# Kernel optimization log

Measured on AMD Instinct MI355X. Metric: run time of the kernel, lower is better.

The kernel has to match this reference:

```python
import jax, jax.numpy as jnp
import numpy as np

E, H, I, K, BLK = 16, 2048, 2048, 4, 32
ALPHA, LIMIT = 1.702, 7.0
T = 1024


def setup_inputs() -> dict:
    key = jax.random.key(0)
    ks = jax.random.split(key, 12)
    f32 = jnp.float32
    return {
        "hidden_states": jax.random.normal(ks[0], (T, H), f32),
        "router_weight": jax.random.normal(ks[1], (E, H), f32) * 0.02,
        "router_bias": jax.random.normal(ks[2], (E,), f32) * 0.02,
        "gate_blocks": jax.random.normal(ks[3], (E, I, H // BLK, BLK), f32),
        "gate_scales": jax.random.uniform(ks[4], (E, I, H // BLK), f32, 0.01, 0.04),
        "gate_bias": jax.random.normal(ks[5], (E, I), f32) * 0.02,
        "up_blocks": jax.random.normal(ks[6], (E, I, H // BLK, BLK), f32),
        "up_scales": jax.random.uniform(ks[7], (E, I, H // BLK), f32, 0.01, 0.04),
        "up_bias": jax.random.normal(ks[8], (E, I), f32) * 0.02,
        "down_blocks": jax.random.normal(ks[9], (E, H, I // BLK, BLK), f32),
        "down_scales": jax.random.uniform(ks[10], (E, H, I // BLK), f32, 0.01, 0.04),
        "down_bias": jax.random.normal(ks[11], (E, H), f32) * 0.02,
    }


def reference(hidden_states, router_weight, router_bias,
              gate_blocks, gate_scales, gate_bias,
              up_blocks, up_scales, up_bias,
              down_blocks, down_scales, down_bias):
    x = hidden_states.reshape(-1, H)              # [T, H]
    t = x.shape[0]

    # --- router: top-k + softmax over top-k, scattered to dense scores ---
    logits = x @ router_weight.T + router_bias    # [T, E]
    topv, topi = jax.lax.top_k(logits, K)         # [T, K]
    topv = jax.nn.softmax(topv, axis=-1)
    scores = jnp.zeros((t, E), x.dtype).at[jnp.arange(t)[:, None], topi].set(topv)

    # --- inline block (mxfp4-style) dequantization: blocks * per-block scale ---
    gate_w = (gate_blocks * gate_scales[..., None]).reshape(E, I, H)
    up_w = (up_blocks * up_scales[..., None]).reshape(E, I, H)
    down_w = (down_blocks * down_scales[..., None]).reshape(E, H, I)

    # --- GptOss GLU experts ---
    g = jnp.einsum('th,eih->eti', x, gate_w) + gate_bias[:, None, :]   # [E, T, I]
    u = jnp.einsum('th,eih->eti', x, up_w) + up_bias[:, None, :]
    g = jnp.minimum(g, LIMIT)
    u = jnp.clip(u, -LIMIT, LIMIT)
    glu = g * jax.nn.sigmoid(g * ALPHA)
    h = (u + 1.0) * glu                                                # [E, T, I]
    o = jnp.einsum('eti,ehi->eth', h, down_w) + down_bias[:, None, :]  # [E, T, H]

    # --- weighted combine by routing scores (zero for unrouted experts) ---
    out = jnp.einsum('eth,te->th', o, scores)
    return out
```

## Files before the change

kernel.cpp:

```cpp
#include <hip/hip_runtime.h>


#define HD 2048
#define ID 2048
#define NE 16
#define NT 1024
#define NTOPK 4
#define NSLOTS (NT * NTOPK)

typedef unsigned short u16;
typedef __attribute__((ext_vector_type(8))) short short8;
typedef __attribute__((ext_vector_type(4))) float f32x4;

__device__ __forceinline__ float bf2f(u16 v) {
    return __uint_as_float(((unsigned)v) << 16);
}
__device__ __forceinline__ u16 f2bf(float f) {
    unsigned u = __float_as_uint(f);
    return (u16)((u + 0x7fffu + ((u >> 16) & 1u)) >> 16);
}

__global__ void router_kernel(const float* __restrict__ x,
                              const float* __restrict__ rw,
                              const float* __restrict__ rb,
                              u16* __restrict__ xb,
                              int* __restrict__ counts,
                              int* __restrict__ topi,
                              float* __restrict__ topv) {
    const int t = blockIdx.x;
    const int lane = threadIdx.x;

    float xr[32];
#pragma unroll
    for (int j = 0; j < 32; ++j) xr[j] = x[(size_t)t * HD + j * 64 + lane];
#pragma unroll
    for (int j = 0; j < 32; ++j) xb[(size_t)t * HD + j * 64 + lane] = f2bf(xr[j]);

    float lg[NE];
#pragma unroll
    for (int e = 0; e < NE; ++e) {
        const float* w = rw + (size_t)e * HD;
        float s = 0.f;
#pragma unroll
        for (int j = 0; j < 32; ++j) s = fmaf(xr[j], w[j * 64 + lane], s);
        for (int off = 32; off > 0; off >>= 1) s += __shfl_xor(s, off);
        lg[e] = s + rb[e];
    }

    if (lane == 0) {
        unsigned used = 0;
        float sv[NTOPK];
        int si[NTOPK];
#pragma unroll
        for (int k = 0; k < NTOPK; ++k) {
            float best = -1e30f;
            int bi = 0;
#pragma unroll
            for (int e = 0; e < NE; ++e) {
                if (!(used & (1u << e)) && lg[e] > best) { best = lg[e]; bi = e; }
            }
            used |= 1u << bi;
            sv[k] = best;
            si[k] = bi;
        }
        const float mx = sv[0];
        float p[NTOPK], sum = 0.f;
#pragma unroll
        for (int k = 0; k < NTOPK; ++k) { p[k] = __expf(sv[k] - mx); sum += p[k]; }
        const float inv = 1.0f / sum;
#pragma unroll
        for (int k = 0; k < NTOPK; ++k) {
            atomicAdd(&counts[si[k]], 1);
            topi[t * NTOPK + k] = si[k];
            topv[t * NTOPK + k] = p[k] * inv;
        }
    }
}

__global__ void bases_kernel(const int* __restrict__ counts, int* __restrict__ bases) {
    if (threadIdx.x == 0) {
        int acc = 0;
#pragma unroll
        for (int e = 0; e < NE; ++e) { bases[e] = acc; acc += counts[e]; }
    }
}

__global__ void assign_kernel(const int* __restrict__ topi, const float* __restrict__ topv,
                              const int* __restrict__ bases, int* __restrict__ cursor,
                              int* __restrict__ tok_slot, float* __restrict__ wgt_slot) {
    const int t = blockIdx.x * 256 + threadIdx.x;
    if (t < NT) {
#pragma unroll
        for (int k = 0; k < NTOPK; ++k) {
            const int e = topi[t * NTOPK + k];
            const int s = atomicAdd(&cursor[e], 1);
            const int slot = bases[e] + s;
            tok_slot[slot] = t;
            wgt_slot[slot] = topv[t * NTOPK + k];
        }
    }
}

__global__ __launch_bounds__(256, 2) void gu_gemm(
    const u16* __restrict__ xb,
    const float* __restrict__ gate_blocks, const float* __restrict__ gate_scales,
    const float* __restrict__ gate_bias,
    const float* __restrict__ up_blocks, const float* __restrict__ up_scales,
    const float* __restrict__ up_bias,
    const int* __restrict__ counts, const int* __restrict__ bases,
    const int* __restrict__ tok_slot,
    u16* __restrict__ gbuf, u16* __restrict__ ubuf) {
    const int e = blockIdx.z >> 1, mat = blockIdx.z & 1;
    const int n_e = counts[e];
    const int mt = blockIdx.y;
    if (mt * 256 >= n_e) return;
    const int rows = min(256, n_e - mt * 256);
    const int base = bases[e] + mt * 256;
    const float* wb = mat ? up_blocks : gate_blocks;
    const float* wsc = mat ? up_scales : gate_scales;
    const float* wbias = mat ? up_bias : gate_bias;
    u16* outb = mat ? ubuf : gbuf;
    const int n0 = blockIdx.x * 64;

    __shared__ __align__(16) short Asl[4][256][8];
    __shared__ __align__(16) short Bsl[4][64][8];

    const int tid = threadIdx.x;
    const int wave = tid >> 6, lane = tid & 63;

    const int tokA = tok_slot[base + min(tid, rows - 1)];
    const u16* aptr = xb + (size_t)tokA * HD;
    const int bn = tid & 63, bq = tid >> 6;
    const float* bptr = wb + ((size_t)e * ID + n0 + bn) * HD + bq * 8;
    const float* sptr = wsc + ((size_t)e * ID + n0 + bn) * (HD / 32);

    f32x4 acc[4][4];
#pragma unroll
    for (int a = 0; a < 4; ++a)
#pragma unroll
        for (int b = 0; b < 4; ++b) acc[a][b] = (f32x4){0.f, 0.f, 0.f, 0.f};

    int4 areg0, areg1, areg2, areg3;
    float4 br0, br1;
    float sreg;
    {
        const int4* ap = (const int4*)aptr;
        areg0 = ap[0]; areg1 = ap[1]; areg2 = ap[2]; areg3 = ap[3];
        const float4* bp = (const float4*)bptr;
        br0 = bp[0]; br1 = bp[1];
        sreg = sptr[0];
    }

    for (int kb = 0; kb < 64; ++kb) {
        __syncthreads();
        *(int4*)&Asl[0][tid][0] = areg0;
        *(int4*)&Asl[1][tid][0] = areg1;
        *(int4*)&Asl[2][tid][0] = areg2;
        *(int4*)&Asl[3][tid][0] = areg3;
        {
            const int p0 = (int)((unsigned)f2bf(br0.x * sreg) | ((unsigned)f2bf(br0.y * sreg) << 16));
            const int p1 = (int)((unsigned)f2bf(br0.z * sreg) | ((unsigned)f2bf(br0.w * sreg) << 16));
            const int p2 = (int)((unsigned)f2bf(br1.x * sreg) | ((unsigned)f2bf(br1.y * sreg) << 16));
            const int p3 = (int)((unsigned)f2bf(br1.z * sreg) | ((unsigned)f2bf(br1.w * sreg) << 16));
            *(int4*)&Bsl[bq][bn][0] = make_int4(p0, p1, p2, p3);
        }
        __syncthreads();
        if (kb < 63) {
            const int4* ap = (const int4*)(aptr + (kb + 1) * 32);
            areg0 = ap[0]; areg1 = ap[1]; areg2 = ap[2]; areg3 = ap[3];
            const float4* bp = (const float4*)(bptr + (kb + 1) * 32);
            br0 = bp[0]; br1 = bp[1];
            sreg = sptr[kb + 1];
        }
        const int kch = lane >> 4, lr = lane & 15;
        short8 af[4], bfv[4];
#pragma unroll
        for (int mi = 0; mi < 4; ++mi)
            af[mi] = *(const short8*)&Asl[kch][wave * 64 + mi * 16 + lr][0];
#pragma unroll
        for (int ni = 0; ni < 4; ++ni)
            bfv[ni] = *(const short8*)&Bsl[kch][ni * 16 + lr][0];
#pragma unroll
        for (int mi = 0; mi < 4; ++mi)
#pragma unroll
            for (int ni = 0; ni < 4; ++ni)
                acc[mi][ni] = __builtin_amdgcn_mfma_f32_16x16x32_bf16(af[mi], bfv[ni], acc[mi][ni], 0, 0, 0);
    }

    const int lr = lane & 15, qq = lane >> 4;
#pragma unroll
    for (int ni = 0; ni < 4; ++ni) {
        const int col = n0 + ni * 16 + lr;
        const float bv = wbias[e * ID + col];
#pragma unroll
        for (int mi = 0; mi < 4; ++mi)
#pragma unroll
            for (int j = 0; j < 4; ++j) {
                const int ml = wave * 64 + mi * 16 + qq * 4 + j;
                if (ml < rows) outb[(size_t)(base + ml) * ID + col] = f2bf(acc[mi][ni][j] + bv);
            }
    }
}

__global__ void act_kernel(const u16* __restrict__ g, const u16* __restrict__ u,
                           u16* __restrict__ h) {
    const size_t i = (size_t)blockIdx.x * 256 + threadIdx.x;
    const int4 gv = ((const int4*)g)[i];
    const int4 uv = ((const int4*)u)[i];
    const int gi[4] = {gv.x, gv.y, gv.z, gv.w};
    const int ui[4] = {uv.x, uv.y, uv.z, uv.w};
    int hi[4];
#pragma unroll
    for (int c = 0; c < 4; ++c) {
        float res[2];
#pragma unroll
        for (int p = 0; p < 2; ++p) {
            float gg = bf2f((u16)(((unsigned)gi[c] >> (16 * p)) & 0xffffu));
            float uu = bf2f((u16)(((unsigned)ui[c] >> (16 * p)) & 0xffffu));
            gg = fminf(gg, 7.0f);
            uu = fminf(fmaxf(uu, -7.0f), 7.0f);
            const float sig = 1.0f / (1.0f + __expf(-1.702f * gg));
            res[p] = (uu + 1.0f) * (gg * sig);
        }
        hi[c] = (int)((unsigned)f2bf(res[0]) | ((unsigned)f2bf(res[1]) << 16));
    }
    ((int4*)h)[i] = make_int4(hi[0], hi[1], hi[2], hi[3]);
}

__global__ __launch_bounds__(256, 2) void down_gemm(
    const u16* __restrict__ hbuf,
    const float* __restrict__ down_blocks, const float* __restrict__ down_scales,
    const float* __restrict__ down_bias,
    const int* __restrict__ counts, const int* __restrict__ bases,
    const int* __restrict__ tok_slot, const float* __restrict__ wgt_slot,
    float* __restrict__ out) {
    const int e = blockIdx.z;
    const int n_e = counts[e];
    const int mt = blockIdx.y;
    if (mt * 256 >= n_e) return;
    const int rows = min(256, n_e - mt * 256);
    const int base = bases[e] + mt * 256;
    const int n0 = blockIdx.x * 64;

    __shared__ __align__(16) short Asl[4][256][8];
    __shared__ __align__(16) short Bsl[4][64][8];

    const int tid = threadIdx.x;
    const int wave = tid >> 6, lane = tid & 63;

    const int slotA = min(base + tid, NSLOTS - 1);
    const u16* aptr = hbuf + (size_t)slotA * ID;
    const int bn = tid & 63, bq = tid >> 6;
    const float* bptr = down_blocks + ((size_t)e * HD + n0 + bn) * ID + bq * 8;
    const float* sptr = down_scales + ((size_t)e * HD + n0 + bn) * (ID / 32);

    f32x4 acc[4][4];
#pragma unroll
    for (int a = 0; a < 4; ++a)
#pragma unroll
        for (int b = 0; b < 4; ++b) acc[a][b] = (f32x4){0.f, 0.f, 0.f, 0.f};

    int4 areg0, areg1, areg2, areg3;
    float4 br0, br1;
    float sreg;
    {
        const int4* ap = (const int4*)aptr;
        areg0 = ap[0]; areg1 = ap[1]; areg2 = ap[2]; areg3 = ap[3];
        const float4* bp = (const float4*)bptr;
        br0 = bp[0]; br1 = bp[1];
        sreg = sptr[0];
    }

    for (int kb = 0; kb < 64; ++kb) {
        __syncthreads();
        *(int4*)&Asl[0][tid][0] = areg0;
        *(int4*)&Asl[1][tid][0] = areg1;
        *(int4*)&Asl[2][tid][0] = areg2;
        *(int4*)&Asl[3][tid][0] = areg3;
        {
            const int p0 = (int)((unsigned)f2bf(br0.x * sreg) | ((unsigned)f2bf(br0.y * sreg) << 16));
            const int p1 = (int)((unsigned)f2bf(br0.z * sreg) | ((unsigned)f2bf(br0.w * sreg) << 16));
            const int p2 = (int)((unsigned)f2bf(br1.x * sreg) | ((unsigned)f2bf(br1.y * sreg) << 16));
            const int p3 = (int)((unsigned)f2bf(br1.z * sreg) | ((unsigned)f2bf(br1.w * sreg) << 16));
            *(int4*)&Bsl[bq][bn][0] = make_int4(p0, p1, p2, p3);
        }
        __syncthreads();
        if (kb < 63) {
            const int4* ap = (const int4*)(aptr + (kb + 1) * 32);
            areg0 = ap[0]; areg1 = ap[1]; areg2 = ap[2]; areg3 = ap[3];
            const float4* bp = (const float4*)(bptr + (kb + 1) * 32);
            br0 = bp[0]; br1 = bp[1];
            sreg = sptr[kb + 1];
        }
        const int kch = lane >> 4, lr = lane & 15;
        short8 af[4], bfv[4];
#pragma unroll
        for (int mi = 0; mi < 4; ++mi)
            af[mi] = *(const short8*)&Asl[kch][wave * 64 + mi * 16 + lr][0];
#pragma unroll
        for (int ni = 0; ni < 4; ++ni)
            bfv[ni] = *(const short8*)&Bsl[kch][ni * 16 + lr][0];
#pragma unroll
        for (int mi = 0; mi < 4; ++mi)
#pragma unroll
            for (int ni = 0; ni < 4; ++ni)
                acc[mi][ni] = __builtin_amdgcn_mfma_f32_16x16x32_bf16(af[mi], bfv[ni], acc[mi][ni], 0, 0, 0);
    }

    const int lr = lane & 15, qq = lane >> 4;
    float bvs[4];
#pragma unroll
    for (int ni = 0; ni < 4; ++ni) bvs[ni] = down_bias[e * HD + n0 + ni * 16 + lr];
#pragma unroll
    for (int mi = 0; mi < 4; ++mi)
#pragma unroll
        for (int j = 0; j < 4; ++j) {
            const int ml = wave * 64 + mi * 16 + qq * 4 + j;
            if (ml >= rows) continue;
            const int slot = base + ml;
            const int tok = tok_slot[slot];
            const float wg = wgt_slot[slot];
            float* orow = out + (size_t)tok * HD;
#pragma unroll
            for (int ni = 0; ni < 4; ++ni)
                atomicAdd(&orow[n0 + ni * 16 + lr], wg * (acc[mi][ni][j] + bvs[ni]));
        }
}

extern "C" void kernel_launch(void* const* d_in, const int* in_sizes, int n_in,
                              void* d_out, int out_size, void* d_ws, size_t ws_size,
                              hipStream_t stream) {
    const float* x           = (const float*)d_in[0];
    const float* rw          = (const float*)d_in[1];
    const float* rb          = (const float*)d_in[2];
    const float* gate_blocks = (const float*)d_in[3];
    const float* gate_scales = (const float*)d_in[4];
    const float* gate_bias   = (const float*)d_in[5];
    const float* up_blocks   = (const float*)d_in[6];
    const float* up_scales   = (const float*)d_in[7];
    const float* up_bias     = (const float*)d_in[8];
    const float* down_blocks = (const float*)d_in[9];
    const float* down_scales = (const float*)d_in[10];
    const float* down_bias   = (const float*)d_in[11];
    float* out = (float*)d_out;

    char* ws = (char*)d_ws;
    u16* xb     = (u16*)ws;
    u16* gbuf   = (u16*)(ws + (4 << 20));
    u16* ubuf   = (u16*)(ws + (20 << 20));
    u16* hbuf   = (u16*)(ws + (36 << 20));
    int* counts = (int*)(ws + (52 << 20));
    int* cursor = counts + 16;
    int* basesp = counts + 32;
    int* topi   = counts + 64;
    float* topv = (float*)(counts + 64 + 4096);
    int* tok_slot = (int*)(counts + 64 + 8192);
    float* wgt_slot = (float*)(counts + 64 + 12288);

    hipMemsetAsync(d_out, 0, (size_t)NT * HD * sizeof(float), stream);
    hipMemsetAsync(counts, 0, 128, stream);

    router_kernel<<<NT, 64, 0, stream>>>(x, rw, rb, xb, counts, topi, topv);
    bases_kernel<<<1, 64, 0, stream>>>(counts, basesp);
    assign_kernel<<<NT / 256, 256, 0, stream>>>(topi, topv, basesp, cursor, tok_slot, wgt_slot);
    gu_gemm<<<dim3(ID / 64, 4, NE * 2), 256, 0, stream>>>(
        xb, gate_blocks, gate_scales, gate_bias, up_blocks, up_scales, up_bias,
        counts, basesp, tok_slot, gbuf, ubuf);
    act_kernel<<<(NSLOTS * ID / 8) / 256, 256, 0, stream>>>(gbuf, ubuf, hbuf);
    down_gemm<<<dim3(HD / 64, 4, NE), 256, 0, stream>>>(
        hbuf, down_blocks, down_scales, down_bias, counts, basesp, tok_slot, wgt_slot, out);
}
```

Baseline: 1.525 ms.

## Load A fragments directly from global and double-buffer dequantized B in LDS

Result: faster. 1.279 ms (-16.1%).

```diff
diff --git a/kernel.cpp b/kernel.cpp
--- a/kernel.cpp
+++ b/kernel.cpp
@@ -122,17 +122,23 @@
     u16* outb = mat ? ubuf : gbuf;
     const int n0 = blockIdx.x * 64;
 
-    __shared__ __align__(16) short Asl[4][256][8];
-    __shared__ __align__(16) short Bsl[4][64][8];
+    __shared__ __align__(16) short Bsl[2][8][64][8];
 
     const int tid = threadIdx.x;
     const int wave = tid >> 6, lane = tid & 63;
-
-    const int tokA = tok_slot[base + min(tid, rows - 1)];
-    const u16* aptr = xb + (size_t)tokA * HD;
-    const int bn = tid & 63, bq = tid >> 6;
-    const float* bptr = wb + ((size_t)e * ID + n0 + bn) * HD + bq * 8;
-    const float* sptr = wsc + ((size_t)e * ID + n0 + bn) * (HD / 32);
+    const int lr = lane & 15, kch = lane >> 4;
+
+    const u16* ap[4];
+#pragma unroll
+    for (int mi = 0; mi < 4; ++mi) {
+        const int m = wave * 64 + mi * 16 + lr;
+        const int tok = tok_slot[base + min(m, rows - 1)];
+        ap[mi] = xb + (size_t)tok * HD + kch * 8;
+    }
+
+    const int col = tid & 63, q = tid >> 6;
+    const float* bptr = wb + ((size_t)e * ID + n0 + col) * HD + q * 16;
+    const float* sptr = wsc + ((size_t)e * ID + n0 + col) * (HD / 32);
 
     f32x4 acc[4][4];
 #pragma unroll
@@ -140,64 +146,78 @@
 #pragma unroll
         for (int b = 0; b < 4; ++b) acc[a][b] = (f32x4){0.f, 0.f, 0.f, 0.f};
 
-    int4 areg0, areg1, areg2, areg3;
-    float4 br0, br1;
-    float sreg;
-    {
-        const int4* ap = (const int4*)aptr;
-        areg0 = ap[0]; areg1 = ap[1]; areg2 = ap[2]; areg3 = ap[3];
-        const float4* bp = (const float4*)bptr;
-        br0 = bp[0]; br1 = bp[1];
-        sreg = sptr[0];
-    }
-
-    for (int kb = 0; kb < 64; ++kb) {
+    float4 br0, br1, br2, br3;
+    float sc;
+#define LOADB(KB)                                                    \
+    {                                                                \
+        const float4* p = (const float4*)(bptr + (KB) * 64);         \
+        br0 = p[0]; br1 = p[1]; br2 = p[2]; br3 = p[3];              \
+        sc = sptr[(KB) * 2 + (q >> 1)];                              \
+    }
+#define WRITEB(BUF)                                                  \
+    {                                                                \
+        short8 lo, hi;                                               \
+        lo[0] = (short)f2bf(br0.x * sc); lo[1] = (short)f2bf(br0.y * sc); \
+        lo[2] = (short)f2bf(br0.z * sc); lo[3] = (short)f2bf(br0.w * sc); \
+        lo[4] = (short)f2bf(br1.x * sc); lo[5] = (short)f2bf(br1.y * sc); \
+        lo[6] = (short)f2bf(br1.z * sc); lo[7] = (short)f2bf(br1.w * sc); \
+        hi[0] = (short)f2bf(br2.x * sc); hi[1] = (short)f2bf(br2.y * sc); \
+        hi[2] = (short)f2bf(br2.z * sc); hi[3] = (short)f2bf(br2.w * sc); \
+        hi[4] = (short)f2bf(br3.x * sc); hi[5] = (short)f2bf(br3.y * sc); \
+        hi[6] = (short)f2bf(br3.z * sc); hi[7] = (short)f2bf(br3.w * sc); \
+        *(short8*)&Bsl[BUF][q * 2][col][0] = lo;                     \
+        *(short8*)&Bsl[BUF][q * 2 + 1][col][0] = hi;                 \
+    }
+
+    LOADB(0);
+    WRITEB(0);
+    LOADB(1);
+    __syncthreads();
+
+    for (int kb = 0; kb < 32; ++kb) {
+        short8 a0[4], a1[4];
+#pragma unroll
+        for (int mi = 0; mi < 4; ++mi) {
+            a0[mi] = *(const short8*)(ap[mi] + kb * 64);
+            a1[mi] = *(const short8*)(ap[mi] + kb * 64 + 32);
+        }
+        if (kb + 1 < 32) {
+            WRITEB((kb + 1) & 1);
+            if (kb + 2 < 32) LOADB(kb + 2);
+        }
+        const int buf = kb & 1;
+        short8 bfv[2][4];
+#pragma unroll
+        for (int s = 0; s < 2; ++s)
+#pragma unroll
+            for (int ni = 0; ni < 4; ++ni)
+                bfv[s][ni] = *(const short8*)&Bsl[buf][s * 4 + kch][ni * 16 + lr][0];
+#pragma unroll
+        for (int mi = 0; mi < 4; ++mi)
+#pragma unroll
+            for (int ni = 0; ni < 4; ++ni)
+                acc[mi][ni] = __builtin_amdgcn_mfma_f32_16x16x32_bf16(a0[mi], bfv[0][ni], acc[mi][ni], 0, 0, 0);
+#pragma unroll
+        for (int mi = 0; mi < 4; ++mi)
+#pragma unroll
+            for (int ni = 0; ni < 4; ++ni)
+                acc[mi][ni] = __builtin_amdgcn_mfma_f32_16x16x32_bf16(a1[mi], bfv[1][ni], acc[mi][ni], 0, 0, 0);
         __syncthreads();
-        *(int4*)&Asl[0][tid][0] = areg0;
-        *(int4*)&Asl[1][tid][0] = areg1;
-        *(int4*)&Asl[2][tid][0] = areg2;
-        *(int4*)&Asl[3][tid][0] = areg3;
-        {
-            const int p0 = (int)((unsigned)f2bf(br0.x * sreg) | ((unsigned)f2bf(br0.y * sreg) << 16));
-            const int p1 = (int)((unsigned)f2bf(br0.z * sreg) | ((unsigned)f2bf(br0.w * sreg) << 16));
-            const int p2 = (int)((unsigned)f2bf(br1.x * sreg) | ((unsigned)f2bf(br1.y * sreg) << 16));
-            const int p3 = (int)((unsigned)f2bf(br1.z * sreg) | ((unsigned)f2bf(br1.w * sreg) << 16));
-            *(int4*)&Bsl[bq][bn][0] = make_int4(p0, p1, p2, p3);
-        }
-        __syncthreads();
-        if (kb < 63) {
-            const int4* ap = (const int4*)(aptr + (kb + 1) * 32);
-            areg0 = ap[0]; areg1 = ap[1]; areg2 = ap[2]; areg3 = ap[3];
-            const float4* bp = (const float4*)(bptr + (kb + 1) * 32);
-            br0 = bp[0]; br1 = bp[1];
-            sreg = sptr[kb + 1];
-        }
-        const int kch = lane >> 4, lr = lane & 15;
-        short8 af[4], bfv[4];
-#pragma unroll
-        for (int mi = 0; mi < 4; ++mi)
-            af[mi] = *(const short8*)&Asl[kch][wave * 64 + mi * 16 + lr][0];
-#pragma unroll
-        for (int ni = 0; ni < 4; ++ni)
-            bfv[ni] = *(const short8*)&Bsl[kch][ni * 16 + lr][0];
-#pragma unroll
-        for (int mi = 0; mi < 4; ++mi)
-#pragma unroll
-            for (int ni = 0; ni < 4; ++ni)
-                acc[mi][ni] = __builtin_amdgcn_mfma_f32_16x16x32_bf16(af[mi], bfv[ni], acc[mi][ni], 0, 0, 0);
-    }
-
-    const int lr = lane & 15, qq = lane >> 4;
+    }
+#undef LOADB
+#undef WRITEB
+
+    const int qq = lane >> 4;
 #pragma unroll
     for (int ni = 0; ni < 4; ++ni) {
-        const int col = n0 + ni * 16 + lr;
-        const float bv = wbias[e * ID + col];
+        const int colo = n0 + ni * 16 + lr;
+        const float bv = wbias[e * ID + colo];
 #pragma unroll
         for (int mi = 0; mi < 4; ++mi)
 #pragma unroll
             for (int j = 0; j < 4; ++j) {
                 const int ml = wave * 64 + mi * 16 + qq * 4 + j;
-                if (ml < rows) outb[(size_t)(base + ml) * ID + col] = f2bf(acc[mi][ni][j] + bv);
+                if (ml < rows) outb[(size_t)(base + ml) * ID + colo] = f2bf(acc[mi][ni][j] + bv);
             }
     }
 }
@@ -242,17 +262,23 @@
     const int base = bases[e] + mt * 256;
     const int n0 = blockIdx.x * 64;
 
-    __shared__ __align__(16) short Asl[4][256][8];
-    __shared__ __align__(16) short Bsl[4][64][8];
+    __shared__ __align__(16) short Bsl[2][8][64][8];
 
     const int tid = threadIdx.x;
     const int wave = tid >> 6, lane = tid & 63;
-
-    const int slotA = min(base + tid, NSLOTS - 1);
-    const u16* aptr = hbuf + (size_t)slotA * ID;
-    const int bn = tid & 63, bq = tid >> 6;
-    const float* bptr = down_blocks + ((size_t)e * HD + n0 + bn) * ID + bq * 8;
-    const float* sptr = down_scales + ((size_t)e * HD + n0 + bn) * (ID / 32);
+    const int lr = lane & 15, kch = lane >> 4;
+
+    const u16* ap[4];
+#pragma unroll
+    for (int mi = 0; mi < 4; ++mi) {
+        const int m = wave * 64 + mi * 16 + lr;
+        const int slot = base + min(m, rows - 1);
+        ap[mi] = hbuf + (size_t)slot * ID + kch * 8;
+    }
+
+    const int col = tid & 63, q = tid >> 6;
+    const float* bptr = down_blocks + ((size_t)e * HD + n0 + col) * ID + q * 16;
+    const float* sptr = down_scales + ((size_t)e * HD + n0 + col) * (ID / 32);
 
     f32x4 acc[4][4];
 #pragma unroll
@@ -260,54 +286,68 @@
 #pragma unroll
         for (int b = 0; b < 4; ++b) acc[a][b] = (f32x4){0.f, 0.f, 0.f, 0.f};
 
-    int4 areg0, areg1, areg2, areg3;
-    float4 br0, br1;
-    float sreg;
-    {
-        const int4* ap = (const int4*)aptr;
-        areg0 = ap[0]; areg1 = ap[1]; areg2 = ap[2]; areg3 = ap[3];
-        const float4* bp = (const float4*)bptr;
-        br0 = bp[0]; br1 = bp[1];
-        sreg = sptr[0];
-    }
-
-    for (int kb = 0; kb < 64; ++kb) {
+    float4 br0, br1, br2, br3;
+    float sc;
+#define LOADB(KB)                                                    \
+    {                                                                \
+        const float4* p = (const float4*)(bptr + (KB) * 64);         \
+        br0 = p[0]; br1 = p[1]; br2 = p[2]; br3 = p[3];              \
+        sc = sptr[(KB) * 2 + (q >> 1)];                              \
+    }
+#define WRITEB(BUF)                                                  \
+    {                                                                \
+        short8 lo, hi;                                               \
+        lo[0] = (short)f2bf(br0.x * sc); lo[1] = (short)f2bf(br0.y * sc); \
+        lo[2] = (short)f2bf(br0.z * sc); lo[3] = (short)f2bf(br0.w * sc); \
+        lo[4] = (short)f2bf(br1.x * sc); lo[5] = (short)f2bf(br1.y * sc); \
+        lo[6] = (short)f2bf(br1.z * sc); lo[7] = (short)f2bf(br1.w * sc); \
+        hi[0] = (short)f2bf(br2.x * sc); hi[1] = (short)f2bf(br2.y * sc); \
+        hi[2] = (short)f2bf(br2.z * sc); hi[3] = (short)f2bf(br2.w * sc); \
+        hi[4] = (short)f2bf(br3.x * sc); hi[5] = (short)f2bf(br3.y * sc); \
+        hi[6] = (short)f2bf(br3.z * sc); hi[7] = (short)f2bf(br3.w * sc); \
+        *(short8*)&Bsl[BUF][q * 2][col][0] = lo;                     \
+        *(short8*)&Bsl[BUF][q * 2 + 1][col][0] = hi;                 \
+    }
+
+    LOADB(0);
+    WRITEB(0);
+    LOADB(1);
+    __syncthreads();
+
+    for (int kb = 0; kb < 32; ++kb) {
+        short8 a0[4], a1[4];
+#pragma unroll
+        for (int mi = 0; mi < 4; ++mi) {
+            a0[mi] = *(const short8*)(ap[mi] + kb * 64);
+            a1[mi] = *(const short8*)(ap[mi] + kb * 64 + 32);
+        }
+        if (kb + 1 < 32) {
+            WRITEB((kb + 1) & 1);
+            if (kb + 2 < 32) LOADB(kb + 2);
+        }
+        const int buf = kb & 1;
+        short8 bfv[2][4];
+#pragma unroll
+        for (int s = 0; s < 2; ++s)
+#pragma unroll
+            for (int ni = 0; ni < 4; ++ni)
+                bfv[s][ni] = *(const short8*)&Bsl[buf][s * 4 + kch][ni * 16 + lr][0];
+#pragma unroll
+        for (int mi = 0; mi < 4; ++mi)
+#pragma unroll
+            for (int ni = 0; ni < 4; ++ni)
+                acc[mi][ni] = __builtin_amdgcn_mfma_f32_16x16x32_bf16(a0[mi], bfv[0][ni], acc[mi][ni], 0, 0, 0);
+#pragma unroll
+        for (int mi = 0; mi < 4; ++mi)
+#pragma unroll
+            for (int ni = 0; ni < 4; ++ni)
+                acc[mi][ni] = __builtin_amdgcn_mfma_f32_16x16x32_bf16(a1[mi], bfv[1][ni], acc[mi][ni], 0, 0, 0);
         __syncthreads();
-        *(int4*)&Asl[0][tid][0] = areg0;
-        *(int4*)&Asl[1][tid][0] = areg1;
-        *(int4*)&Asl[2][tid][0] = areg2;
-        *(int4*)&Asl[3][tid][0] = areg3;
-        {
-            const int p0 = (int)((unsigned)f2bf(br0.x * sreg) | ((unsigned)f2bf(br0.y * sreg) << 16));
-            const int p1 = (int)((unsigned)f2bf(br0.z * sreg) | ((unsigned)f2bf(br0.w * sreg) << 16));
-            const int p2 = (int)((unsigned)f2bf(br1.x * sreg) | ((unsigned)f2bf(br1.y * sreg) << 16));
-            const int p3 = (int)((unsigned)f2bf(br1.z * sreg) | ((unsigned)f2bf(br1.w * sreg) << 16));
-            *(int4*)&Bsl[bq][bn][0] = make_int4(p0, p1, p2, p3);
-        }
-        __syncthreads();
-        if (kb < 63) {
-            const int4* ap = (const int4*)(aptr + (kb + 1) * 32);
-            areg0 = ap[0]; areg1 = ap[1]; areg2 = ap[2]; areg3 = ap[3];
-            const float4* bp = (const float4*)(bptr + (kb + 1) * 32);
-            br0 = bp[0]; br1 = bp[1];
-            sreg = sptr[kb + 1];
-        }
-        const int kch = lane >> 4, lr = lane & 15;
-        short8 af[4], bfv[4];
-#pragma unroll
-        for (int mi = 0; mi < 4; ++mi)
-            af[mi] = *(const short8*)&Asl[kch][wave * 64 + mi * 16 + lr][0];
-#pragma unroll
-        for (int ni = 0; ni < 4; ++ni)
-            bfv[ni] = *(const short8*)&Bsl[kch][ni * 16 + lr][0];
-#pragma unroll
-        for (int mi = 0; mi < 4; ++mi)
-#pragma unroll
-            for (int ni = 0; ni < 4; ++ni)
-                acc[mi][ni] = __builtin_amdgcn_mfma_f32_16x16x32_bf16(af[mi], bfv[ni], acc[mi][ni], 0, 0, 0);
-    }
-
-    const int lr = lane & 15, qq = lane >> 4;
+    }
+#undef LOADB
+#undef WRITEB
+
+    const int qq = lane >> 4;
     float bvs[4];
 #pragma unroll
     for (int ni = 0; ni < 4; ++ni) bvs[ni] = down_bias[e * HD + n0 + ni * 16 + lr];
```
